# Optimization experiments

Hardware: AMD Instinct MI355X
Metric: run time of the kernel (lower is better)

## Reference

```python
import jax, jax.numpy as jnp
import numpy as np

N = 50000   # number_of_nodes
E = 800000  # edges
K = 3       # Chebyshev order
C_IN = 64
C_OUT = 64


def _laplacian_weights(src, dst, w):
    # PyG ChebConv sym normalization with lambda_max=2: L_hat = -D^{-1/2} A D^{-1/2}
    deg = jax.ops.segment_sum(w, src, num_segments=N)
    dis = jnp.where(deg > 0, jax.lax.rsqrt(jnp.maximum(deg, 1e-12)), 0.0)
    return -dis[src] * w * dis[dst]


def _cheb(x, src, dst, lw, W, b):
    # x: [N, Cin], W: [K, Cin, Cout], b: [Cout]
    def prop(t):  # sparse L_hat @ t via gather + segment-sum scatter
        return jax.ops.segment_sum(lw[:, None] * t[src], dst, num_segments=N)
    Tx0 = x
    out = Tx0 @ W[0]
    Tx1 = prop(Tx0)
    out = out + Tx1 @ W[1]
    for k in range(2, W.shape[0]):  # Chebyshev recursion T_k = 2 L T_{k-1} - T_{k-2}
        Tx2 = 2.0 * prop(Tx1) - Tx0
        out = out + Tx2 @ W[k]
        Tx0, Tx1 = Tx1, Tx2
    return out + b


def setup_inputs() -> dict:
    key = jax.random.key(0)
    ks = jax.random.split(key, 20)
    inp = {
        "X": jax.random.normal(ks[0], (N, C_IN), jnp.float32),
        "edge_index": jax.random.randint(ks[1], (2, E), 0, N, jnp.int64),
        "edge_weight": jax.random.uniform(ks[2], (E,), jnp.float32),
        "H": jax.random.normal(ks[3], (N, C_OUT), jnp.float32),
    }
    names = ["xz", "hz", "xr", "hr", "xh", "hh"]
    for i, n in enumerate(names):
        cin = C_IN if n[0] == "x" else C_OUT
        inp[f"W_{n}"] = 0.1 * jax.random.normal(ks[4 + i], (K, cin, C_OUT), jnp.float32)
        inp[f"b_{n}"] = 0.1 * jax.random.normal(ks[10 + i], (C_OUT,), jnp.float32)
    return inp


def reference(X, edge_index, edge_weight, H,
              W_xz, W_hz, W_xr, W_hr, W_xh, W_hh,
              b_xz, b_hz, b_xr, b_hr, b_xh, b_hh):
    src, dst = edge_index[0], edge_index[1]
    lw = _laplacian_weights(src, dst, edge_weight)
    Z = jax.nn.sigmoid(_cheb(X, src, dst, lw, W_xz, b_xz) +
                       _cheb(H, src, dst, lw, W_hz, b_hz))
    R = jax.nn.sigmoid(_cheb(X, src, dst, lw, W_xr, b_xr) +
                       _cheb(H, src, dst, lw, W_hr, b_hr))
    H_tilde = jnp.tanh(_cheb(X, src, dst, lw, W_xh, b_xh) +
                       _cheb(H * R, src, dst, lw, W_hh, b_hh))
    H_new = Z * H + (1.0 - Z) * H_tilde
    return H_new
```

## Files before the change

### kernel.cpp

```cpp
#include <hip/hip_runtime.h>
#include <math.h>

#define CH 64

typedef __attribute__((ext_vector_type(8))) short bf16x8;
typedef __attribute__((ext_vector_type(4))) float f32x4;

static __device__ __forceinline__ float bf2f(ushort u) {
    union { unsigned int i; float f; } v; v.i = ((unsigned int)u) << 16; return v.f;
}
static __device__ __forceinline__ ushort f2bf(float f) {
    union { float f; unsigned int i; } v; v.f = f;
    unsigned int lsb = (v.i >> 16) & 1;
    v.i += 0x7fffu + lsb;
    return (ushort)(v.i >> 16);
}
static __device__ __forceinline__ unsigned int pack2(float a, float b) {
    return (unsigned int)f2bf(a) | ((unsigned int)f2bf(b) << 16);
}
static __device__ __forceinline__ float lo16(unsigned int u) { return bf2f((ushort)(u & 0xffffu)); }
static __device__ __forceinline__ float hi16(unsigned int u) { return bf2f((ushort)(u >> 16)); }


__global__ __launch_bounds__(256) void k_init(
    const int* __restrict__ src, const int* __restrict__ dst,
    const float* __restrict__ w,
    float* __restrict__ deg, int* __restrict__ cnt, int* __restrict__ erank, int E,
    const float4* __restrict__ X, const float4* __restrict__ H,
    ushort* __restrict__ XHb, int total4,
    const float* __restrict__ Wxz, const float* __restrict__ Whz,
    const float* __restrict__ Wxr, const float* __restrict__ Whr,
    const float* __restrict__ Wxh, const float* __restrict__ Whh,
    ushort* __restrict__ Bp, int bE, int bC)
{
    int b = blockIdx.x;
    int tid = threadIdx.x;
    if (b < bE) {
        int i = b * 256 + tid;
        if (i < E) {
            atomicAdd(&deg[src[i]], w[i]);
            erank[i] = atomicAdd(&cnt[dst[i]], 1);
        }
    } else if (b < bE + bC) {
        int i = (b - bE) * 256 + tid;
        if (i < total4) {
            float4 x = X[i], h = H[i];
            int node = i >> 4, c4 = i & 15;
            ushort4 xb, hb;
            xb.x = f2bf(x.x); xb.y = f2bf(x.y); xb.z = f2bf(x.z); xb.w = f2bf(x.w);
            hb.x = f2bf(h.x); hb.y = f2bf(h.y); hb.z = f2bf(h.z); hb.w = f2bf(h.w);
            *(ushort4*)(XHb + (size_t)node * 128 + c4 * 4)      = xb;
            *(ushort4*)(XHb + (size_t)node * 128 + 64 + c4 * 4) = hb;
        }
    } else {
        int mtg = b - bE - bC;
        int ct = tid >> 6;
        int lane = tid & 63;
        const float* W; int m, kt;
        if (mtg < 12)      { int l = mtg;      m = l >> 1; kt = l & 1; W = (m < 3) ? Wxz + m * 4096 : Whz + (m - 3) * 4096; }
        else if (mtg < 24) { int l = mtg - 12; m = l >> 1; kt = l & 1; W = (m < 3) ? Wxr + m * 4096 : Whr + (m - 3) * 4096; }
        else if (mtg < 30) { int l = mtg - 24; m = l >> 1; kt = l & 1; W = Wxh + m * 4096; }
        else               { int l = mtg - 30; m = l >> 1; kt = l & 1; W = Whh + m * 4096; }
        int cout = ct * 16 + (lane & 15);
        ushort* dstp = Bp + ((((mtg * 4) + ct) * 64 + lane) << 3);
        #pragma unroll
        for (int e = 0; e < 8; ++e) {
            int cin = kt * 32 + ((lane >> 4) << 3) + e;
            dstp[e] = f2bf(W[cin * 64 + cout]);
        }
    }
}


__global__ __launch_bounds__(256) void k_scanA(const int* __restrict__ cnt,
                                               int* __restrict__ rowptr,
                                               int* __restrict__ bsum, int N) {
    __shared__ int ts[256];
    int tid = threadIdx.x;
    int base = blockIdx.x * 2048 + tid * 8;
    int v[8]; int s = 0;
    #pragma unroll
    for (int k = 0; k < 8; ++k) { int i = base + k; v[k] = (i < N) ? cnt[i] : 0; s += v[k]; }
    ts[tid] = s;
    __syncthreads();
    for (int off = 1; off < 256; off <<= 1) {
        int t = (tid >= off) ? ts[tid - off] : 0;
        __syncthreads();
        ts[tid] += t;
        __syncthreads();
    }
    int run = ts[tid] - s;
    #pragma unroll
    for (int k = 0; k < 8; ++k) { int i = base + k; if (i < N) rowptr[i] = run; run += v[k]; }
    if (tid == 255) bsum[blockIdx.x] = ts[255];
}

__global__ void k_scanB(int* __restrict__ bsum, int B) {
    if (threadIdx.x == 0) {
        int acc = 0;
        for (int b = 0; b < B; ++b) { int t = bsum[b]; bsum[b] = acc; acc += t; }
        bsum[B] = acc;
    }
}

__global__ __launch_bounds__(256) void k_scanC(int* __restrict__ rowptr,
                                               const int* __restrict__ bsum,
                                               float* __restrict__ deg, int N, int B) {
    int base = blockIdx.x * 2048 + threadIdx.x * 8;
    int add = bsum[blockIdx.x];
    #pragma unroll
    for (int k = 0; k < 8; ++k) {
        int i = base + k;
        if (i < N) {
            rowptr[i] += add;
            float d = deg[i];
            deg[i] = (d > 0.f) ? rsqrtf(fmaxf(d, 1e-12f)) : 0.f;
        }
    }
    if (blockIdx.x == 0 && threadIdx.x == 0) rowptr[N] = bsum[B];
}


__global__ __launch_bounds__(256) void k_scatter(const int* __restrict__ src,
                                                 const int* __restrict__ dst,
                                                 const float* __restrict__ w,
                                                 const float* __restrict__ dis,
                                                 const int* __restrict__ rowptr,
                                                 const int* __restrict__ erank,
                                                 int2* __restrict__ emeta, int E) {
    int e = blockIdx.x * 256 + threadIdx.x;
    if (e < E) {
        int d = dst[e], s = src[e];
        int pos = rowptr[d] + erank[e];
        float lw = -dis[s] * w[e] * dis[d];
        emeta[pos] = make_int2(s, __float_as_int(lw));
    }
}


__global__ __launch_bounds__(256) void k_prop_dual(const int* __restrict__ rowptr,
                                                   const int2* __restrict__ emeta,
                                                   const unsigned int* __restrict__ t,
                                                   unsigned int* __restrict__ o, int N) {
    int wid = (blockIdx.x * 256 + threadIdx.x) >> 6;
    int lane = threadIdx.x & 63;
    if (wid >= N) return;
    int beg = rowptr[wid], end = rowptr[wid + 1];
    float ax = 0.f, ay = 0.f;
    int j = beg;
    for (; j + 3 < end; j += 4) {
        int2 m0 = emeta[j], m1 = emeta[j + 1], m2 = emeta[j + 2], m3 = emeta[j + 3];
        unsigned int p0 = t[(size_t)m0.x * 64 + lane];
        unsigned int p1 = t[(size_t)m1.x * 64 + lane];
        unsigned int p2 = t[(size_t)m2.x * 64 + lane];
        unsigned int p3 = t[(size_t)m3.x * 64 + lane];
        float l0 = __int_as_float(m0.y), l1 = __int_as_float(m1.y);
        float l2 = __int_as_float(m2.y), l3 = __int_as_float(m3.y);
        ax = fmaf(l0, lo16(p0), ax); ay = fmaf(l0, hi16(p0), ay);
        ax = fmaf(l1, lo16(p1), ax); ay = fmaf(l1, hi16(p1), ay);
        ax = fmaf(l2, lo16(p2), ax); ay = fmaf(l2, hi16(p2), ay);
        ax = fmaf(l3, lo16(p3), ax); ay = fmaf(l3, hi16(p3), ay);
    }
    for (; j < end; ++j) {
        int2 m = emeta[j];
        unsigned int p = t[(size_t)m.x * 64 + lane];
        float l = __int_as_float(m.y);
        ax = fmaf(l, lo16(p), ax); ay = fmaf(l, hi16(p), ay);
    }
    o[(size_t)wid * 64 + lane] = pack2(ax, ay);
}

__global__ __launch_bounds__(256) void k_prop_dual2(const int* __restrict__ rowptr,
                                                    const int2* __restrict__ emeta,
                                                    const unsigned int* __restrict__ t,
                                                    const unsigned int* __restrict__ t0,
                                                    unsigned int* __restrict__ o, int N) {
    int wid = (blockIdx.x * 256 + threadIdx.x) >> 6;
    int lane = threadIdx.x & 63;
    if (wid >= N) return;
    int beg = rowptr[wid], end = rowptr[wid + 1];
    float ax = 0.f, ay = 0.f;
    int j = beg;
    for (; j + 3 < end; j += 4) {
        int2 m0 = emeta[j], m1 = emeta[j + 1], m2 = emeta[j + 2], m3 = emeta[j + 3];
        unsigned int p0 = t[(size_t)m0.x * 64 + lane];
        unsigned int p1 = t[(size_t)m1.x * 64 + lane];
        unsigned int p2 = t[(size_t)m2.x * 64 + lane];
        unsigned int p3 = t[(size_t)m3.x * 64 + lane];
        float l0 = __int_as_float(m0.y), l1 = __int_as_float(m1.y);
        float l2 = __int_as_float(m2.y), l3 = __int_as_float(m3.y);
        ax = fmaf(l0, lo16(p0), ax); ay = fmaf(l0, hi16(p0), ay);
        ax = fmaf(l1, lo16(p1), ax); ay = fmaf(l1, hi16(p1), ay);
        ax = fmaf(l2, lo16(p2), ax); ay = fmaf(l2, hi16(p2), ay);
        ax = fmaf(l3, lo16(p3), ax); ay = fmaf(l3, hi16(p3), ay);
    }
    for (; j < end; ++j) {
        int2 m = emeta[j];
        unsigned int p = t[(size_t)m.x * 64 + lane];
        float l = __int_as_float(m.y);
        ax = fmaf(l, lo16(p), ax); ay = fmaf(l, hi16(p), ay);
    }
    size_t oi = (size_t)wid * 64 + lane;
    unsigned int z = t0[oi];
    o[oi] = pack2(2.f * ax - lo16(z), 2.f * ay - hi16(z));
}


__global__ __launch_bounds__(256) void k_prop1(const int* __restrict__ rowptr,
                                               const int2* __restrict__ emeta,
                                               const unsigned int* __restrict__ t,
                                               unsigned int* __restrict__ out, int N) {
    int wv = (blockIdx.x * 256 + threadIdx.x) >> 6;
    int lane = threadIdx.x & 63;
    int node = wv * 2 + (lane >> 5);
    int sl = lane & 31;
    if (node >= N) return;
    int beg = rowptr[node], end = rowptr[node + 1];
    float ax = 0.f, ay = 0.f;
    int j = beg;
    for (; j + 3 < end; j += 4) {
        int2 m0 = emeta[j], m1 = emeta[j + 1], m2 = emeta[j + 2], m3 = emeta[j + 3];
        unsigned int p0 = t[(size_t)m0.x * 32 + sl];
        unsigned int p1 = t[(size_t)m1.x * 32 + sl];
        unsigned int p2 = t[(size_t)m2.x * 32 + sl];
        unsigned int p3 = t[(size_t)m3.x * 32 + sl];
        float l0 = __int_as_float(m0.y), l1 = __int_as_float(m1.y);
        float l2 = __int_as_float(m2.y), l3 = __int_as_float(m3.y);
        ax = fmaf(l0, lo16(p0), ax); ay = fmaf(l0, hi16(p0), ay);
        ax = fmaf(l1, lo16(p1), ax); ay = fmaf(l1, hi16(p1), ay);
        ax = fmaf(l2, lo16(p2), ax); ay = fmaf(l2, hi16(p2), ay);
        ax = fmaf(l3, lo16(p3), ax); ay = fmaf(l3, hi16(p3), ay);
    }
    for (; j < end; ++j) {
        int2 m = emeta[j];
        unsigned int p = t[(size_t)m.x * 32 + sl];
        float l = __int_as_float(m.y);
        ax = fmaf(l, lo16(p), ax); ay = fmaf(l, hi16(p), ay);
    }
    out[(size_t)node * 32 + sl] = pack2(ax, ay);
}

__global__ __launch_bounds__(256) void k_prop2(const int* __restrict__ rowptr,
                                               const int2* __restrict__ emeta,
                                               const unsigned int* __restrict__ t,
                                               const unsigned int* __restrict__ t0,
                                               unsigned int* __restrict__ out, int N) {
    int wv = (blockIdx.x * 256 + threadIdx.x) >> 6;
    int lane = threadIdx.x & 63;
    int node = wv * 2 + (lane >> 5);
    int sl = lane & 31;
    if (node >= N) return;
    int beg = rowptr[node], end = rowptr[node + 1];
    float ax = 0.f, ay = 0.f;
    int j = beg;
    for (; j + 3 < end; j += 4) {
        int2 m0 = emeta[j], m1 = emeta[j + 1], m2 = emeta[j + 2], m3 = emeta[j + 3];
        unsigned int p0 = t[(size_t)m0.x * 32 + sl];
        unsigned int p1 = t[(size_t)m1.x * 32 + sl];
        unsigned int p2 = t[(size_t)m2.x * 32 + sl];
        unsigned int p3 = t[(size_t)m3.x * 32 + sl];
        float l0 = __int_as_float(m0.y), l1 = __int_as_float(m1.y);
        float l2 = __int_as_float(m2.y), l3 = __int_as_float(m3.y);
        ax = fmaf(l0, lo16(p0), ax); ay = fmaf(l0, hi16(p0), ay);
        ax = fmaf(l1, lo16(p1), ax); ay = fmaf(l1, hi16(p1), ay);
        ax = fmaf(l2, lo16(p2), ax); ay = fmaf(l2, hi16(p2), ay);
        ax = fmaf(l3, lo16(p3), ax); ay = fmaf(l3, hi16(p3), ay);
    }
    for (; j < end; ++j) {
        int2 m = emeta[j];
        unsigned int p = t[(size_t)m.x * 32 + sl];
        float l = __int_as_float(m.y);
        ax = fmaf(l, lo16(p), ax); ay = fmaf(l, hi16(p), ay);
    }
    size_t oi = (size_t)node * 32 + sl;
    unsigned int z = t0[oi];
    out[oi] = pack2(2.f * ax - lo16(z), 2.f * ay - hi16(z));
}


static __device__ __forceinline__ bf16x8 ldA(const ushort* __restrict__ t, int stride,
                                             int row0, int lane, int kt, int N) {
    int row = row0 + (lane & 15);
    bf16x8 v = {};
    if (row < N) v = *(const bf16x8*)(t + (size_t)row * stride + kt * 32 + ((lane >> 4) << 3));
    return v;
}
static __device__ __forceinline__ bf16x8 ldB(const ushort* __restrict__ bp,
                                             int mt, int ct, int lane) {
    return *(const bf16x8*)(bp + ((((mt * 4) + ct) * 64 + lane) << 3));
}

#define MFMA(a, b, c) __builtin_amdgcn_mfma_f32_16x16x32_bf16(a, b, c, 0, 0, 0)


__global__ __launch_bounds__(256) void k_gA(
    const ushort* __restrict__ XHb, const ushort* __restrict__ T1xh, const ushort* __restrict__ T2xh,
    const ushort* __restrict__ Bp,
    const float* __restrict__ bxz, const float* __restrict__ bhz,
    const float* __restrict__ bxr, const float* __restrict__ bhr,
    const float* __restrict__ bxh,
    const float* __restrict__ H,
    ushort* __restrict__ Zb, ushort* __restrict__ HRb, float* __restrict__ preH, int N)
{
    int wid = blockIdx.x * 4 + (threadIdx.x >> 6);
    int lane = threadIdx.x & 63;
    int row0 = wid * 32;
    if (row0 >= N) return;

    f32x4 accZ[2][4], accR[2][4], accH[2][4];
    #pragma unroll
    for (int ct = 0; ct < 4; ++ct) {
        int col = ct * 16 + (lane & 15);
        float bz = bxz[col] + bhz[col];
        float br = bxr[col] + bhr[col];
        float bh = bxh[col];
        #pragma unroll
        for (int rt = 0; rt < 2; ++rt) {
            accZ[rt][ct] = (f32x4){bz, bz, bz, bz};
            accR[rt][ct] = (f32x4){br, br, br, br};
            accH[rt][ct] = (f32x4){bh, bh, bh, bh};
        }
    }

    const ushort* ins[6] = { XHb, T1xh, T2xh, XHb + 64, T1xh + 64, T2xh + 64 };

    #pragma unroll
    for (int m = 0; m < 6; ++m) {
        #pragma unroll
        for (int kt = 0; kt < 2; ++kt) {
            bf16x8 a0 = ldA(ins[m], 128, row0,      lane, kt, N);
            bf16x8 a1 = ldA(ins[m], 128, row0 + 16, lane, kt, N);
            int mt = m * 2 + kt;
            #pragma unroll
            for (int ct = 0; ct < 4; ++ct) {
                bf16x8 bz8 = ldB(Bp, mt, ct, lane);
                accZ[0][ct] = MFMA(a0, bz8, accZ[0][ct]);
                accZ[1][ct] = MFMA(a1, bz8, accZ[1][ct]);
                bf16x8 br8 = ldB(Bp, 12 + mt, ct, lane);
                accR[0][ct] = MFMA(a0, br8, accR[0][ct]);
                accR[1][ct] = MFMA(a1, br8, accR[1][ct]);
                if (m < 3) {
                    bf16x8 bh8 = ldB(Bp, 24 + mt, ct, lane);
                    accH[0][ct] = MFMA(a0, bh8, accH[0][ct]);
                    accH[1][ct] = MFMA(a1, bh8, accH[1][ct]);
                }
            }
        }
    }

    #pragma unroll
    for (int rt = 0; rt < 2; ++rt) {
        #pragma unroll
        for (int ct = 0; ct < 4; ++ct) {
            int col = ct * 16 + (lane & 15);
            #pragma unroll
            for (int r = 0; r < 4; ++r) {
                int row = row0 + rt * 16 + ((lane >> 4) << 2) + r;
                if (row < N) {
                    int o = row * CH + col;
                    float z = 1.f / (1.f + expf(-accZ[rt][ct][r]));
                    float rr = 1.f / (1.f + expf(-accR[rt][ct][r]));
                    float h = H[o];
                    Zb[o] = f2bf(z);
                    HRb[o] = f2bf(h * rr);
                    preH[o] = accH[rt][ct][r];
                }
            }
        }
    }
}


__global__ __launch_bounds__(256) void k_gB(
    const ushort* __restrict__ HRb, const ushort* __restrict__ T1, const ushort* __restrict__ T2,
    const ushort* __restrict__ Bp, const float* __restrict__ bhh,
    const ushort* __restrict__ Zb, const float* __restrict__ H,
    float* __restrict__ out , int N)
{
    int wid = blockIdx.x * 4 + (threadIdx.x >> 6);
    int lane = threadIdx.x & 63;
    int row0 = wid * 32;
    if (row0 >= N) return;

    f32x4 acc[2][4];
    #pragma unroll
    for (int ct = 0; ct < 4; ++ct) {
        int col = ct * 16 + (lane & 15);
        float bh = bhh[col];
        #pragma unroll
        for (int rt = 0; rt < 2; ++rt) acc[rt][ct] = (f32x4){bh, bh, bh, bh};
    }

    const ushort* ins[3] = { HRb, T1, T2 };

    #pragma unroll
    for (int m = 0; m < 3; ++m) {
        #pragma unroll
        for (int kt = 0; kt < 2; ++kt) {
            bf16x8 a0 = ldA(ins[m], 64, row0,      lane, kt, N);
            bf16x8 a1 = ldA(ins[m], 64, row0 + 16, lane, kt, N);
            int mt = 30 + m * 2 + kt;
            #pragma unroll
            for (int ct = 0; ct < 4; ++ct) {
                bf16x8 b8 = ldB(Bp, mt, ct, lane);
                acc[0][ct] = MFMA(a0, b8, acc[0][ct]);
                acc[1][ct] = MFMA(a1, b8, acc[1][ct]);
            }
        }
    }

    #pragma unroll
    for (int rt = 0; rt < 2; ++rt) {
        #pragma unroll
        for (int ct = 0; ct < 4; ++ct) {
            int col = ct * 16 + (lane & 15);
            #pragma unroll
            for (int r = 0; r < 4; ++r) {
                int row = row0 + rt * 16 + ((lane >> 4) << 2) + r;
                if (row < N) {
                    int o = row * CH + col;
                    float pre = acc[rt][ct][r] + out[o];
                    float z = bf2f(Zb[o]);
                    float h = H[o];
                    out[o] = z * h + (1.f - z) * tanhf(pre);
                }
            }
        }
    }
}


extern "C" void kernel_launch(void* const* d_in, const int* in_sizes, int n_in,
                              void* d_out, int out_size, void* d_ws, size_t ws_size,
                              hipStream_t stream) {
    const float* X   = (const float*)d_in[0];
    const int*   ei  = (const int*)d_in[1];
    const float* ew  = (const float*)d_in[2];
    const float* H   = (const float*)d_in[3];
    const float* Wxz = (const float*)d_in[4];
    const float* bxz = (const float*)d_in[5];
    const float* Whz = (const float*)d_in[6];
    const float* bhz = (const float*)d_in[7];
    const float* Wxr = (const float*)d_in[8];
    const float* bxr = (const float*)d_in[9];
    const float* Whr = (const float*)d_in[10];
    const float* bhr = (const float*)d_in[11];
    const float* Wxh = (const float*)d_in[12];
    const float* bxh = (const float*)d_in[13];
    const float* Whh = (const float*)d_in[14];
    const float* bhh = (const float*)d_in[15];

    const int N = in_sizes[0] / CH;
    const int E = in_sizes[2];
    const long long NC = (long long)N * CH;

    const int* srcI = ei;
    const int* dstI = ei + E;

    char* p = (char*)d_ws;
    auto alloc = [&](size_t bytes) { char* r = p; p += (bytes + 255) & ~(size_t)255; return r; };
    int*    rowptr = (int*)alloc((size_t)(N + 1) * 4);
    int2*   emeta  = (int2*)alloc((size_t)E * 8);
    int*    erank  = (int*)alloc((size_t)E * 4);
    float*  deg    = (float*)alloc((size_t)N * 8);
    int*    cnt    = (int*)(deg + N);
    int*    bsum   = (int*)alloc(256 * 4);
    ushort* Bp     = (ushort*)alloc((size_t)36 * 4 * 64 * 8 * 2);
    ushort* XHb    = (ushort*)alloc((size_t)NC * 2 * 2);
    ushort* T1xh   = (ushort*)alloc((size_t)NC * 2 * 2);
    ushort* T2xh   = (ushort*)alloc((size_t)NC * 2 * 2);
    ushort* HRb    = (ushort*)alloc((size_t)NC * 2);
    ushort* T1r    = (ushort*)alloc((size_t)NC * 2);
    ushort* T2r    = (ushort*)alloc((size_t)NC * 2);
    ushort* Zb     = (ushort*)alloc((size_t)NC * 2);
    float*  preH   = (float*)d_out;

    const int total4 = (int)(NC / 4);
    const int bE = (E + 255) / 256;
    const int bC = (total4 + 255) / 256;
    const int B  = (N + 2047) / 2048;
    const int bW = (int)((N * 64 + 255) / 256);
    const int bW2 = (int)((((N + 1) / 2) * 64 + 255) / 256);
    const int nW = (N + 31) / 32;
    const int bG = (nW + 3) / 4;

    hipMemsetAsync(deg, 0, (size_t)N * 8, stream);
    k_init<<<bE + bC + 36, 256, 0, stream>>>(srcI, dstI, ew, deg, cnt, erank, E,
                                             (const float4*)X, (const float4*)H, XHb, total4,
                                             Wxz, Whz, Wxr, Whr, Wxh, Whh, Bp, bE, bC);

    k_scanA<<<B, 256, 0, stream>>>(cnt, rowptr, bsum, N);
    k_scanB<<<1, 64, 0, stream>>>(bsum, B);
    k_scanC<<<B, 256, 0, stream>>>(rowptr, bsum, deg, N, B);

    k_scatter<<<bE, 256, 0, stream>>>(srcI, dstI, ew, deg, rowptr, erank, emeta, E);

    k_prop_dual <<<bW, 256, 0, stream>>>(rowptr, emeta, (const unsigned int*)XHb,
                                         (unsigned int*)T1xh, N);
    k_prop_dual2<<<bW, 256, 0, stream>>>(rowptr, emeta, (const unsigned int*)T1xh,
                                         (const unsigned int*)XHb, (unsigned int*)T2xh, N);

    k_gA<<<bG, 256, 0, stream>>>(XHb, T1xh, T2xh, Bp,
                                 bxz, bhz, bxr, bhr, bxh,
                                 H, Zb, HRb, preH, N);

    k_prop1<<<bW2, 256, 0, stream>>>(rowptr, emeta, (const unsigned int*)HRb,
                                     (unsigned int*)T1r, N);
    k_prop2<<<bW2, 256, 0, stream>>>(rowptr, emeta, (const unsigned int*)T1r,
                                     (const unsigned int*)HRb, (unsigned int*)T2r, N);

    k_gB<<<bG, 256, 0, stream>>>(HRb, T1r, T2r, Bp, bhh, Zb, H, (float*)d_out, N);
}
```

Baseline: 297.3 us.

## Slice feature buffers into 16-channel planes and gather edges in parallel

Feature tensors are stored as 16-channel slices laid out plane by plane ([slice][node][16]), so each SpMM block handles one slice. That shrinks the gathered working set per pass and should improve cache locality. The propagation kernel now has each wavefront process 8 edges at once (8 lanes per edge, 8 channel-pairs each) and reduce across lanes with xor shuffles, replacing one edge at a time over 64 lanes. The init conversion goes through LDS to write the sliced layout, and the GEMM kernels read A tiles from slices. The costs are extra shuffle reductions, eight times as many blocks, and repeated reads of rowptr and emeta for every slice.

```diff
diff --git a/kernel.cpp b/kernel.cpp
--- a/kernel.cpp
+++ b/kernel.cpp
@@ -26,13 +26,14 @@
     const int* __restrict__ src, const int* __restrict__ dst,
     const float* __restrict__ w,
     float* __restrict__ deg, int* __restrict__ cnt, int* __restrict__ erank, int E,
-    const float4* __restrict__ X, const float4* __restrict__ H,
-    ushort* __restrict__ XHb, int total4,
+    const float4* __restrict__ X4, const float4* __restrict__ H4,
+    ushort* __restrict__ XHs, int N,
     const float* __restrict__ Wxz, const float* __restrict__ Whz,
     const float* __restrict__ Wxr, const float* __restrict__ Whr,
     const float* __restrict__ Wxh, const float* __restrict__ Whh,
     ushort* __restrict__ Bp, int bE, int bC)
 {
+    __shared__ ushort lds[16][128];
     int b = blockIdx.x;
     int tid = threadIdx.x;
     if (b < bE) {
@@ -42,15 +43,29 @@
             erank[i] = atomicAdd(&cnt[dst[i]], 1);
         }
     } else if (b < bE + bC) {
-        int i = (b - bE) * 256 + tid;
-        if (i < total4) {
-            float4 x = X[i], h = H[i];
-            int node = i >> 4, c4 = i & 15;
-            ushort4 xb, hb;
-            xb.x = f2bf(x.x); xb.y = f2bf(x.y); xb.z = f2bf(x.z); xb.w = f2bf(x.w);
-            hb.x = f2bf(h.x); hb.y = f2bf(h.y); hb.z = f2bf(h.z); hb.w = f2bf(h.w);
-            *(ushort4*)(XHb + (size_t)node * 128 + c4 * 4)      = xb;
-            *(ushort4*)(XHb + (size_t)node * 128 + 64 + c4 * 4) = hb;
+        int node0 = (b - bE) * 16;
+        #pragma unroll
+        for (int it = 0; it < 2; ++it) {
+            int fi = it * 256 + tid;
+            int nl = fi >> 5, piece = fi & 31;
+            int node = node0 + nl;
+            if (node < N) {
+                float4 v = (piece < 16) ? X4[(size_t)node * 16 + piece]
+                                        : H4[(size_t)node * 16 + (piece - 16)];
+                ushort4 u;
+                u.x = f2bf(v.x); u.y = f2bf(v.y); u.z = f2bf(v.z); u.w = f2bf(v.w);
+                int ch4 = (piece < 16) ? piece * 4 : 64 + (piece - 16) * 4;
+                *(ushort4*)&lds[nl][ch4] = u;
+            }
+        }
+        __syncthreads();
+        {
+            int slice = tid >> 5, nl = (tid >> 1) & 15, half = tid & 1;
+            int node = node0 + nl;
+            if (node < N) {
+                *(uint4*)(XHs + ((size_t)slice * N + node) * 16 + half * 8) =
+                    *(const uint4*)&lds[nl][slice * 16 + half * 8];
+            }
         }
     } else {
         int mtg = b - bE - bC;
@@ -138,151 +153,53 @@
 }
 
 
-__global__ __launch_bounds__(256) void k_prop_dual(const int* __restrict__ rowptr,
-                                                   const int2* __restrict__ emeta,
-                                                   const unsigned int* __restrict__ t,
-                                                   unsigned int* __restrict__ o, int N) {
-    int wid = (blockIdx.x * 256 + threadIdx.x) >> 6;
+template<int CHEB>
+__global__ __launch_bounds__(256) void k_prop(const int* __restrict__ rowptr,
+                                              const int2* __restrict__ emeta,
+                                              const unsigned int* __restrict__ t,
+                                              const unsigned int* __restrict__ t0,
+                                              unsigned int* __restrict__ o,
+                                              int N, int NS) {
+    int s = blockIdx.x % NS;
+    int n = (blockIdx.x / NS) * 4 + (threadIdx.x >> 6);
+    if (n >= N) return;
     int lane = threadIdx.x & 63;
-    if (wid >= N) return;
-    int beg = rowptr[wid], end = rowptr[wid + 1];
+    int e8 = lane >> 3, c = lane & 7;
+    const unsigned int* tb = t + (size_t)s * N * 8;
+    int beg = rowptr[n], end = rowptr[n + 1];
     float ax = 0.f, ay = 0.f;
-    int j = beg;
-    for (; j + 3 < end; j += 4) {
-        int2 m0 = emeta[j], m1 = emeta[j + 1], m2 = emeta[j + 2], m3 = emeta[j + 3];
-        unsigned int p0 = t[(size_t)m0.x * 64 + lane];
-        unsigned int p1 = t[(size_t)m1.x * 64 + lane];
-        unsigned int p2 = t[(size_t)m2.x * 64 + lane];
-        unsigned int p3 = t[(size_t)m3.x * 64 + lane];
-        float l0 = __int_as_float(m0.y), l1 = __int_as_float(m1.y);
-        float l2 = __int_as_float(m2.y), l3 = __int_as_float(m3.y);
-        ax = fmaf(l0, lo16(p0), ax); ay = fmaf(l0, hi16(p0), ay);
-        ax = fmaf(l1, lo16(p1), ax); ay = fmaf(l1, hi16(p1), ay);
-        ax = fmaf(l2, lo16(p2), ax); ay = fmaf(l2, hi16(p2), ay);
-        ax = fmaf(l3, lo16(p3), ax); ay = fmaf(l3, hi16(p3), ay);
-    }
-    for (; j < end; ++j) {
-        int2 m = emeta[j];
-        unsigned int p = t[(size_t)m.x * 64 + lane];
-        float l = __int_as_float(m.y);
-        ax = fmaf(l, lo16(p), ax); ay = fmaf(l, hi16(p), ay);
-    }
-    o[(size_t)wid * 64 + lane] = pack2(ax, ay);
-}
-
-__global__ __launch_bounds__(256) void k_prop_dual2(const int* __restrict__ rowptr,
-                                                    const int2* __restrict__ emeta,
-                                                    const unsigned int* __restrict__ t,
-                                                    const unsigned int* __restrict__ t0,
-                                                    unsigned int* __restrict__ o, int N) {
-    int wid = (blockIdx.x * 256 + threadIdx.x) >> 6;
-    int lane = threadIdx.x & 63;
-    if (wid >= N) return;
-    int beg = rowptr[wid], end = rowptr[wid + 1];
-    float ax = 0.f, ay = 0.f;
-    int j = beg;
-    for (; j + 3 < end; j += 4) {
-        int2 m0 = emeta[j], m1 = emeta[j + 1], m2 = emeta[j + 2], m3 = emeta[j + 3];
-        unsigned int p0 = t[(size_t)m0.x * 64 + lane];
-        unsigned int p1 = t[(size_t)m1.x * 64 + lane];
-        unsigned int p2 = t[(size_t)m2.x * 64 + lane];
-        unsigned int p3 = t[(size_t)m3.x * 64 + lane];
-        float l0 = __int_as_float(m0.y), l1 = __int_as_float(m1.y);
-        float l2 = __int_as_float(m2.y), l3 = __int_as_float(m3.y);
-        ax = fmaf(l0, lo16(p0), ax); ay = fmaf(l0, hi16(p0), ay);
-        ax = fmaf(l1, lo16(p1), ax); ay = fmaf(l1, hi16(p1), ay);
-        ax = fmaf(l2, lo16(p2), ax); ay = fmaf(l2, hi16(p2), ay);
-        ax = fmaf(l3, lo16(p3), ax); ay = fmaf(l3, hi16(p3), ay);
-    }
-    for (; j < end; ++j) {
-        int2 m = emeta[j];
-        unsigned int p = t[(size_t)m.x * 64 + lane];
-        float l = __int_as_float(m.y);
-        ax = fmaf(l, lo16(p), ax); ay = fmaf(l, hi16(p), ay);
-    }
-    size_t oi = (size_t)wid * 64 + lane;
-    unsigned int z = t0[oi];
-    o[oi] = pack2(2.f * ax - lo16(z), 2.f * ay - hi16(z));
-}
-
-
-__global__ __launch_bounds__(256) void k_prop1(const int* __restrict__ rowptr,
-                                               const int2* __restrict__ emeta,
-                                               const unsigned int* __restrict__ t,
-                                               unsigned int* __restrict__ out, int N) {
-    int wv = (blockIdx.x * 256 + threadIdx.x) >> 6;
-    int lane = threadIdx.x & 63;
-    int node = wv * 2 + (lane >> 5);
-    int sl = lane & 31;
-    if (node >= N) return;
-    int beg = rowptr[node], end = rowptr[node + 1];
-    float ax = 0.f, ay = 0.f;
-    int j = beg;
-    for (; j + 3 < end; j += 4) {
-        int2 m0 = emeta[j], m1 = emeta[j + 1], m2 = emeta[j + 2], m3 = emeta[j + 3];
-        unsigned int p0 = t[(size_t)m0.x * 32 + sl];
-        unsigned int p1 = t[(size_t)m1.x * 32 + sl];
-        unsigned int p2 = t[(size_t)m2.x * 32 + sl];
-        unsigned int p3 = t[(size_t)m3.x * 32 + sl];
-        float l0 = __int_as_float(m0.y), l1 = __int_as_float(m1.y);
-        float l2 = __int_as_float(m2.y), l3 = __int_as_float(m3.y);
-        ax = fmaf(l0, lo16(p0), ax); ay = fmaf(l0, hi16(p0), ay);
-        ax = fmaf(l1, lo16(p1), ax); ay = fmaf(l1, hi16(p1), ay);
-        ax = fmaf(l2, lo16(p2), ax); ay = fmaf(l2, hi16(p2), ay);
-        ax = fmaf(l3, lo16(p3), ax); ay = fmaf(l3, hi16(p3), ay);
-    }
-    for (; j < end; ++j) {
-        int2 m = emeta[j];
-        unsigned int p = t[(size_t)m.x * 32 + sl];
-        float l = __int_as_float(m.y);
-        ax = fmaf(l, lo16(p), ax); ay = fmaf(l, hi16(p), ay);
-    }
-    out[(size_t)node * 32 + sl] = pack2(ax, ay);
-}
-
-__global__ __launch_bounds__(256) void k_prop2(const int* __restrict__ rowptr,
-                                               const int2* __restrict__ emeta,
-                                               const unsigned int* __restrict__ t,
-                                               const unsigned int* __restrict__ t0,
-                                               unsigned int* __restrict__ out, int N) {
-    int wv = (blockIdx.x * 256 + threadIdx.x) >> 6;
-    int lane = threadIdx.x & 63;
-    int node = wv * 2 + (lane >> 5);
-    int sl = lane & 31;
-    if (node >= N) return;
-    int beg = rowptr[node], end = rowptr[node + 1];
-    float ax = 0.f, ay = 0.f;
-    int j = beg;
-    for (; j + 3 < end; j += 4) {
-        int2 m0 = emeta[j], m1 = emeta[j + 1], m2 = emeta[j + 2], m3 = emeta[j + 3];
-        unsigned int p0 = t[(size_t)m0.x * 32 + sl];
-        unsigned int p1 = t[(size_t)m1.x * 32 + sl];
-        unsigned int p2 = t[(size_t)m2.x * 32 + sl];
-        unsigned int p3 = t[(size_t)m3.x * 32 + sl];
-        float l0 = __int_as_float(m0.y), l1 = __int_as_float(m1.y);
-        float l2 = __int_as_float(m2.y), l3 = __int_as_float(m3.y);
-        ax = fmaf(l0, lo16(p0), ax); ay = fmaf(l0, hi16(p0), ay);
-        ax = fmaf(l1, lo16(p1), ax); ay = fmaf(l1, hi16(p1), ay);
-        ax = fmaf(l2, lo16(p2), ax); ay = fmaf(l2, hi16(p2), ay);
-        ax = fmaf(l3, lo16(p3), ax); ay = fmaf(l3, hi16(p3), ay);
-    }
-    for (; j < end; ++j) {
-        int2 m = emeta[j];
-        unsigned int p = t[(size_t)m.x * 32 + sl];
-        float l = __int_as_float(m.y);
-        ax = fmaf(l, lo16(p), ax); ay = fmaf(l, hi16(p), ay);
-    }
-    size_t oi = (size_t)node * 32 + sl;
-    unsigned int z = t0[oi];
-    out[oi] = pack2(2.f * ax - lo16(z), 2.f * ay - hi16(z));
-}
-
-
-static __device__ __forceinline__ bf16x8 ldA(const ushort* __restrict__ t, int stride,
-                                             int row0, int lane, int kt, int N) {
-    int row = row0 + (lane & 15);
+    for (int j0 = beg; j0 < end; j0 += 8) {
+        int j = j0 + e8;
+        if (j < end) {
+            int2 m = emeta[j];
+            unsigned int p = tb[(size_t)m.x * 8 + c];
+            float l = __int_as_float(m.y);
+            ax = fmaf(l, lo16(p), ax);
+            ay = fmaf(l, hi16(p), ay);
+        }
+    }
+    #pragma unroll
+    for (int mask = 8; mask < 64; mask <<= 1) {
+        ax += __shfl_xor(ax, mask, 64);
+        ay += __shfl_xor(ay, mask, 64);
+    }
+    if (e8 == 0) {
+        size_t oi = ((size_t)s * N + n) * 8 + c;
+        if (CHEB) {
+            unsigned int z = t0[oi];
+            o[oi] = pack2(2.f * ax - lo16(z), 2.f * ay - hi16(z));
+        } else {
+            o[oi] = pack2(ax, ay);
+        }
+    }
+}
+
+
+static __device__ __forceinline__ bf16x8 ldA_s(const ushort* __restrict__ base,
+                                               int N, int row, int gch) {
     bf16x8 v = {};
-    if (row < N) v = *(const bf16x8*)(t + (size_t)row * stride + kt * 32 + ((lane >> 4) << 3));
+    if (row < N)
+        v = *(const bf16x8*)(base + ((size_t)(gch >> 4) * N + row) * 16 + (gch & 15));
     return v;
 }
 static __device__ __forceinline__ bf16x8 ldB(const ushort* __restrict__ bp,
@@ -294,13 +211,13 @@
 
 
 __global__ __launch_bounds__(256) void k_gA(
-    const ushort* __restrict__ XHb, const ushort* __restrict__ T1xh, const ushort* __restrict__ T2xh,
+    const ushort* __restrict__ XHs, const ushort* __restrict__ T1s, const ushort* __restrict__ T2s,
     const ushort* __restrict__ Bp,
     const float* __restrict__ bxz, const float* __restrict__ bhz,
     const float* __restrict__ bxr, const float* __restrict__ bhr,
     const float* __restrict__ bxh,
     const float* __restrict__ H,
-    ushort* __restrict__ Zb, ushort* __restrict__ HRb, float* __restrict__ preH, int N)
+    ushort* __restrict__ Zb, ushort* __restrict__ HRs, float* __restrict__ preH, int N)
 {
     int wid = blockIdx.x * 4 + (threadIdx.x >> 6);
     int lane = threadIdx.x & 63;
@@ -322,14 +239,17 @@
         }
     }
 
-    const ushort* ins[6] = { XHb, T1xh, T2xh, XHb + 64, T1xh + 64, T2xh + 64 };
+    const ushort* bufs[3] = { XHs, T1s, T2s };
 
     #pragma unroll
     for (int m = 0; m < 6; ++m) {
+        const ushort* buf = bufs[m < 3 ? m : m - 3];
+        int gofs = (m < 3) ? 0 : 64;
         #pragma unroll
         for (int kt = 0; kt < 2; ++kt) {
-            bf16x8 a0 = ldA(ins[m], 128, row0,      lane, kt, N);
-            bf16x8 a1 = ldA(ins[m], 128, row0 + 16, lane, kt, N);
+            int gch = gofs + kt * 32 + ((lane >> 4) << 3);
+            bf16x8 a0 = ldA_s(buf, N, row0 + (lane & 15), gch);
+            bf16x8 a1 = ldA_s(buf, N, row0 + 16 + (lane & 15), gch);
             int mt = m * 2 + kt;
             #pragma unroll
             for (int ct = 0; ct < 4; ++ct) {
@@ -362,7 +282,7 @@
                     float rr = 1.f / (1.f + expf(-accR[rt][ct][r]));
                     float h = H[o];
                     Zb[o] = f2bf(z);
-                    HRb[o] = f2bf(h * rr);
+                    HRs[((size_t)ct * N + row) * 16 + (lane & 15)] = f2bf(h * rr);
                     preH[o] = accH[rt][ct][r];
                 }
             }
@@ -372,7 +292,7 @@
 
 
 __global__ __launch_bounds__(256) void k_gB(
-    const ushort* __restrict__ HRb, const ushort* __restrict__ T1, const ushort* __restrict__ T2,
+    const ushort* __restrict__ HRs, const ushort* __restrict__ T1r, const ushort* __restrict__ T2r,
     const ushort* __restrict__ Bp, const float* __restrict__ bhh,
     const ushort* __restrict__ Zb, const float* __restrict__ H,
     float* __restrict__ out , int N)
@@ -391,14 +311,15 @@
         for (int rt = 0; rt < 2; ++rt) acc[rt][ct] = (f32x4){bh, bh, bh, bh};
     }
 
-    const ushort* ins[3] = { HRb, T1, T2 };
+    const ushort* bufs[3] = { HRs, T1r, T2r };
 
     #pragma unroll
     for (int m = 0; m < 3; ++m) {
         #pragma unroll
         for (int kt = 0; kt < 2; ++kt) {
-            bf16x8 a0 = ldA(ins[m], 64, row0,      lane, kt, N);
-            bf16x8 a1 = ldA(ins[m], 64, row0 + 16, lane, kt, N);
+            int gch = kt * 32 + ((lane >> 4) << 3);
+            bf16x8 a0 = ldA_s(bufs[m], N, row0 + (lane & 15), gch);
+            bf16x8 a1 = ldA_s(bufs[m], N, row0 + 16 + (lane & 15), gch);
             int mt = 30 + m * 2 + kt;
             #pragma unroll
             for (int ct = 0; ct < 4; ++ct) {
@@ -466,27 +387,26 @@
     int*    cnt    = (int*)(deg + N);
     int*    bsum   = (int*)alloc(256 * 4);
     ushort* Bp     = (ushort*)alloc((size_t)36 * 4 * 64 * 8 * 2);
-    ushort* XHb    = (ushort*)alloc((size_t)NC * 2 * 2);
-    ushort* T1xh   = (ushort*)alloc((size_t)NC * 2 * 2);
-    ushort* T2xh   = (ushort*)alloc((size_t)NC * 2 * 2);
-    ushort* HRb    = (ushort*)alloc((size_t)NC * 2);
+    ushort* XHs    = (ushort*)alloc((size_t)NC * 2 * 2);
+    ushort* T1s    = (ushort*)alloc((size_t)NC * 2 * 2);
+    ushort* T2s    = (ushort*)alloc((size_t)NC * 2 * 2);
+    ushort* HRs    = (ushort*)alloc((size_t)NC * 2);
     ushort* T1r    = (ushort*)alloc((size_t)NC * 2);
     ushort* T2r    = (ushort*)alloc((size_t)NC * 2);
     ushort* Zb     = (ushort*)alloc((size_t)NC * 2);
     float*  preH   = (float*)d_out;
 
-    const int total4 = (int)(NC / 4);
     const int bE = (E + 255) / 256;
-    const int bC = (total4 + 255) / 256;
+    const int bC = (N + 15) / 16;
     const int B  = (N + 2047) / 2048;
-    const int bW = (int)((N * 64 + 255) / 256);
-    const int bW2 = (int)((((N + 1) / 2) * 64 + 255) / 256);
+    const int bP8 = 8 * ((N + 3) / 4);
+    const int bP4 = 4 * ((N + 3) / 4);
     const int nW = (N + 31) / 32;
     const int bG = (nW + 3) / 4;
 
     hipMemsetAsync(deg, 0, (size_t)N * 8, stream);
     k_init<<<bE + bC + 36, 256, 0, stream>>>(srcI, dstI, ew, deg, cnt, erank, E,
-                                             (const float4*)X, (const float4*)H, XHb, total4,
+                                             (const float4*)X, (const float4*)H, XHs, N,
                                              Wxz, Whz, Wxr, Whr, Wxh, Whh, Bp, bE, bC);
 
     k_scanA<<<B, 256, 0, stream>>>(cnt, rowptr, bsum, N);
@@ -495,19 +415,19 @@
 
     k_scatter<<<bE, 256, 0, stream>>>(srcI, dstI, ew, deg, rowptr, erank, emeta, E);
 
-    k_prop_dual <<<bW, 256, 0, stream>>>(rowptr, emeta, (const unsigned int*)XHb,
-                                         (unsigned int*)T1xh, N);
-    k_prop_dual2<<<bW, 256, 0, stream>>>(rowptr, emeta, (const unsigned int*)T1xh,
-                                         (const unsigned int*)XHb, (unsigned int*)T2xh, N);
-
-    k_gA<<<bG, 256, 0, stream>>>(XHb, T1xh, T2xh, Bp,
+    k_prop<0><<<bP8, 256, 0, stream>>>(rowptr, emeta, (const unsigned int*)XHs,
+                                       (const unsigned int*)XHs, (unsigned int*)T1s, N, 8);
+    k_prop<1><<<bP8, 256, 0, stream>>>(rowptr, emeta, (const unsigned int*)T1s,
+                                       (const unsigned int*)XHs, (unsigned int*)T2s, N, 8);
+
+    k_gA<<<bG, 256, 0, stream>>>(XHs, T1s, T2s, Bp,
                                  bxz, bhz, bxr, bhr, bxh,
-                                 H, Zb, HRb, preH, N);
-
-    k_prop1<<<bW2, 256, 0, stream>>>(rowptr, emeta, (const unsigned int*)HRb,
-                                     (unsigned int*)T1r, N);
-    k_prop2<<<bW2, 256, 0, stream>>>(rowptr, emeta, (const unsigned int*)T1r,
-                                     (const unsigned int*)HRb, (unsigned int*)T2r, N);
-
-    k_gB<<<bG, 256, 0, stream>>>(HRb, T1r, T2r, Bp, bhh, Zb, H, (float*)d_out, N);
-}
+                                 H, Zb, HRs, preH, N);
+
+    k_prop<0><<<bP4, 256, 0, stream>>>(rowptr, emeta, (const unsigned int*)HRs,
+                                       (const unsigned int*)HRs, (unsigned int*)T1r, N, 4);
+    k_prop<1><<<bP4, 256, 0, stream>>>(rowptr, emeta, (const unsigned int*)T1r,
+                                       (const unsigned int*)HRs, (unsigned int*)T2r, N, 4);
+
+    k_gB<<<bG, 256, 0, stream>>>(HRs, T1r, T2r, Bp, bhh, Zb, H, (float*)d_out, N);
+}
```

Measured after the change: 536.9 us. +80.6%, slower.
